# Kernel tuning notes

Measured on AMD Instinct MI355X. Metric: run time of the kernel, lower is better.

## Reference

```python
import jax, jax.numpy as jnp
import numpy as np

N, NN, NI, ND, NH = 20000, 32, 128, 128, 8
RADIUS = 1.0
EPS = 1e-5


def _mlp(x, W1, b1, W2, b2):
    return jax.nn.elu(x @ W1 + b1) @ W2 + b2


def setup_inputs() -> dict:
    key = jax.random.key(0)
    ks = jax.random.split(key, 32)
    s = 0.05
    inp = {
        "features": jax.random.normal(ks[0], (N, NI), jnp.float32),
        "x": jax.random.normal(ks[1], (N, 3), jnp.float32),
        "nuv": jax.random.normal(ks[2], (N, 3, 3), jnp.float32),
        "topk": jax.random.randint(ks[3], (N, NN), 0, N, jnp.int64),
        # query_f: Ni -> Nd -> Nh*Nd
        "qW1": jax.random.normal(ks[4], (NI, ND), jnp.float32) * s,
        "qb1": jnp.zeros((ND,), jnp.float32),
        "qW2": jax.random.normal(ks[5], (ND, NH * ND), jnp.float32) * s,
        "qb2": jnp.zeros((NH * ND,), jnp.float32),
        # geo_encoder: 12 -> Nd -> Nd
        "gW1": jax.random.normal(ks[6], (12, ND), jnp.float32) * s,
        "gb1": jnp.zeros((ND,), jnp.float32),
        "gW2": jax.random.normal(ks[7], (ND, ND), jnp.float32) * s,
        "gb2": jnp.zeros((ND,), jnp.float32),
        # key_f / value_f: Nd -> Nd -> Nd
        "kW1": jax.random.normal(ks[8], (ND, ND), jnp.float32) * s,
        "kb1": jnp.zeros((ND,), jnp.float32),
        "kW2": jax.random.normal(ks[9], (ND, ND), jnp.float32) * s,
        "kb2": jnp.zeros((ND,), jnp.float32),
        "vW1": jax.random.normal(ks[10], (ND, ND), jnp.float32) * s,
        "vb1": jnp.zeros((ND,), jnp.float32),
        "vW2": jax.random.normal(ks[11], (ND, ND), jnp.float32) * s,
        "vb2": jnp.zeros((ND,), jnp.float32),
        # decode_f: Nh*Nd -> Nd -> Nd
        "dW1": jax.random.normal(ks[12], (NH * ND, ND), jnp.float32) * s,
        "db1": jnp.zeros((ND,), jnp.float32),
        "dW2": jax.random.normal(ks[13], (ND, ND), jnp.float32) * s,
        "db2": jnp.zeros((ND,), jnp.float32),
        # LayerNorm
        "ln_g": jnp.ones((ND,), jnp.float32),
        "ln_b": jnp.zeros((ND,), jnp.float32),
    }
    return inp


def reference(features, x, nuv, topk, qW1, qb1, qW2, qb2, gW1, gb1, gW2, gb2,
              kW1, kb1, kW2, kb2, vW1, vb1, vW2, vb2, dW1, db1, dW2, db2,
              ln_g, ln_b):
    n, nn = topk.shape
    sdk = jnp.sqrt(jnp.float32(ND))

    Q = _mlp(features, qW1, qb1, qW2, qb2).reshape(n, NH, ND)  # (N,Nh,Nd)

    features_nn = features[topk]              # (N,nn,Nd)
    x_nn = x[topk]                            # (N,nn,3)
    orient_x = x_nn - x[:, None, :]           # (N,nn,3)
    nuv_nn = nuv[topk].reshape(n, nn * 3, 3)  # (N,nn*3,3)

    dis2 = jnp.sum(orient_x * orient_x, axis=2, keepdims=True)
    dis = jnp.exp(-dis2 / (2.0 * RADIUS * RADIUS))  # (N,nn,1)

    # rotate neighbor offsets / frames into local frame: nuv @ v^T, then transpose
    RL_x = jnp.einsum('nij,nkj->nki', nuv, orient_x)            # (N,nn,3)
    RL_nuv = jnp.einsum('nij,nkj->nki', nuv, nuv_nn)            # (N,nn*3,3)
    RL_nuv = RL_nuv.reshape(n, nn, 9)
    RL = jnp.concatenate([RL_x, RL_nuv], axis=-1)               # (N,nn,12)

    geo_fea = _mlp(RL, gW1, gb1, gW2, gb2)
    geo_fea = dis * geo_fea * features_nn                       # (N,nn,Nd)

    K = _mlp(geo_fea, kW1, kb1, kW2, kb2)                       # (N,nn,Nd)
    V = _mlp(geo_fea, vW1, vb1, vW2, vb2)                       # (N,nn,Nd)

    Mq = jnp.einsum('nhd,nkd->nhk', Q, K)                       # (N,Nh,nn)
    mask = (topk == 0)[:, None, :]                              # (N,1,nn)
    Mq = jnp.where(mask, -jnp.inf, Mq)
    Mq = jax.nn.softmax(Mq / sdk, axis=2)

    out = jnp.einsum('nhk,nkd->nhd', Mq, V).reshape(n, NH * ND)
    out = _mlp(out, dW1, db1, dW2, db2) + features

    mu = jnp.mean(out, axis=-1, keepdims=True)
    var = jnp.var(out, axis=-1, keepdims=True)
    return (out - mu) / jnp.sqrt(var + EPS) * ln_g + ln_b
```

## Files before the change

kernel.cpp:

```cpp
#include <hip/hip_runtime.h>
#include <math.h>
#include <stdint.h>

#define ND 128
#define NNB 32
#define NH 8

typedef __attribute__((ext_vector_type(8))) short bf16x8;
typedef __attribute__((ext_vector_type(4))) float f32x4;
typedef __attribute__((ext_vector_type(8))) unsigned short u16x8;
typedef __attribute__((ext_vector_type(2))) unsigned int u32x2;
typedef unsigned short u16;
typedef unsigned int u32;
typedef unsigned long long u64;

#define OFF_QW1T 0ULL
#define OFF_QW2T 32768ULL
#define OFF_GW1T 294912ULL
#define OFF_GW2T 303104ULL
#define OFF_KW1T 335872ULL
#define OFF_KW2T 368640ULL
#define OFF_VW1T 401408ULL
#define OFF_VW2T 434176ULL
#define OFF_DW1T 466944ULL
#define OFF_DW2T 729088ULL
#define OFF_Q    761856ULL
#define OFF_ATT  (OFF_Q + 20096ULL * 2048ULL)

#define SBAR() asm volatile("s_waitcnt lgkmcnt(0)\n\ts_barrier" ::: "memory")

__device__ __forceinline__ u16 rneb(float f){
    u32 u = __builtin_bit_cast(u32, f);
    u32 r = u + 0x7fffu + ((u >> 16) & 1u);
    return (u16)(r >> 16);
}
__device__ __forceinline__ float elu_f(float v){ return v > 0.f ? v : (__expf(v) - 1.f); }

__device__ __forceinline__ u32 cvtpk(float a, float b){
    u32 r;
    asm("v_cvt_pk_bf16_f32 %0, %1, %2" : "=v"(r) : "v"(a), "v"(b));
    return r;
}
__device__ __forceinline__ u32x2 cvt4(float a, float b, float c, float d){
    u32x2 r; r.x = cvtpk(a, b); r.y = cvtpk(c, d); return r;
}

#define GLDS16(g, l) __builtin_amdgcn_global_load_lds( \
    (const __attribute__((address_space(1))) u32*)(g), \
    (__attribute__((address_space(3))) u32*)(u32)(u64)(l), 16, 0, 0)

__device__ __forceinline__ bf16x8 ldfrag(const u16* base, int row, int kb, int l){
    int r = row + (l & 15);
    int byte = (r << 8) + (((kb << 1) + ((l >> 4) << 4)) ^ ((r & 7) << 4));
    return *(const bf16x8*)((const char*)base + byte);
}
__device__ __forceinline__ bf16x8 ldfragRL(const u16* base, int row, int l){
    int r = row + (l & 15);
    int byte = (r << 6) + ((((l >> 4) << 4)) ^ ((r & 3) << 4));
    return *(const bf16x8*)((const char*)base + byte);
}
__device__ __forceinline__ bf16x8 ldfragG(const char* __restrict__ Wt, int n, int kstride, int kb, int l){
    return *(const bf16x8*)(Wt + (size_t)(n + (l & 15)) * (size_t)kstride
                               + (size_t)((kb << 1) + ((l >> 4) << 4)));
}

__device__ __forceinline__ void gemm2x4(const char* __restrict__ Wt, int kstride, int kbase,
                                        const u16* B, f32x4 acc[2][4], int m0, int n0, int l){
    bf16x8 aw[4][2];
    #pragma unroll
    for (int kk = 0; kk < 4; kk++)
        #pragma unroll
        for (int i = 0; i < 2; i++)
            aw[kk][i] = ldfragG(Wt, m0 + i * 16, kstride, kbase + kk * 32, l);
    __builtin_amdgcn_s_setprio(1);
    #pragma unroll
    for (int kk = 0; kk < 4; kk++){
        #pragma unroll
        for (int nt = 0; nt < 4; nt++){
            bf16x8 b = ldfrag(B, n0 + nt * 16, kk * 32, l);
            #pragma unroll
            for (int mt = 0; mt < 2; mt++)
                acc[mt][nt] = __builtin_amdgcn_mfma_f32_16x16x32_bf16(aw[kk][mt], b, acc[mt][nt], 0, 0, 0);
        }
    }
    __builtin_amdgcn_s_setprio(0);
}

__device__ __forceinline__ void bias_init2(f32x4 acc[2][4], const float* __restrict__ bias,
                                           int m0, int hi){
    #pragma unroll
    for (int mt = 0; mt < 2; mt++){
        float4 bq = *(const float4*)&bias[m0 + mt * 16 + (hi << 2)];
        #pragma unroll
        for (int nt = 0; nt < 4; nt++)
            acc[mt][nt] = (f32x4){bq.x, bq.y, bq.z, bq.w};
    }
}

struct PrepDesc {
    const float* src[10];
    u64 dstoff[10];
    int N[10], Ksrc[10], Kdst[10];
};

__global__ __launch_bounds__(256) void prep_weights(PrepDesc d, char* ws){
    int tid = blockIdx.x * 256 + threadIdx.x;
    #pragma unroll 1
    for (int m = 0; m < 10; m++){
        int cnt = (d.Kdst[m] * d.N[m]) >> 3;
        if (tid < cnt){
            int N = d.N[m];
            int nn = tid % N, k8 = tid / N;
            const float* s = d.src[m];
            u16x8 pk;
            #pragma unroll
            for (int i = 0; i < 8; i++){
                int k = k8 * 8 + i;
                pk[i] = (k < d.Ksrc[m]) ? rneb(s[(size_t)k * N + nn]) : (u16)0;
            }
            *(u16x8*)(ws + d.dstoff[m] + (u64)nn * (u64)(d.Kdst[m] * 2) + (u64)(k8 * 16)) = pk;
            return;
        }
        tid -= cnt;
    }
}

__global__ __launch_bounds__(512, 2) void qmlp_kernel(
    const float* __restrict__ F, const float* __restrict__ qb1, const float* __restrict__ qb2,
    const char* __restrict__ ws, u16* __restrict__ Qg, int n)
{
    __shared__ __align__(16) u16 sIn[16384];
    __shared__ __align__(16) u16 sH[16384];
    const int t = threadIdx.x;
    const int row0 = blockIdx.x * 128;
    const int l = t & 63, w = t >> 6;
    const int m0 = (w & 3) * 32, n0 = (w >> 2) * 64;
    const int hi = l >> 4;

    for (int i = t; i < 4096; i += 512){
        int r = i >> 5, c = (i & 31) * 4;
        int gr = row0 + r;
        float4 v = make_float4(0.f, 0.f, 0.f, 0.f);
        if (gr < n) v = *(const float4*)&F[(size_t)gr * ND + c];
        *(u32x2*)((char*)sIn + (r << 8) + (((c << 1)) ^ ((r & 7) << 4))) = cvt4(v.x, v.y, v.z, v.w);
    }
    SBAR();

    {
        f32x4 acc[2][4];
        bias_init2(acc, qb1, m0, hi);
        gemm2x4(ws + OFF_QW1T, 256, 0, sIn, acc, m0, n0, l);
        #pragma unroll
        for (int mt = 0; mt < 2; mt++){
            int ch0 = m0 + mt * 16 + (hi << 2);
            #pragma unroll
            for (int nt = 0; nt < 4; nt++){
                int row = n0 + nt * 16 + (l & 15);
                *(u32x2*)((char*)sH + (row << 8) + (((ch0 << 1)) ^ ((row & 7) << 4))) =
                    cvt4(elu_f(acc[mt][nt][0]), elu_f(acc[mt][nt][1]),
                         elu_f(acc[mt][nt][2]), elu_f(acc[mt][nt][3]));
            }
        }
    }
    SBAR();

    for (int ct = 0; ct < 8; ct++){
        f32x4 a2[2][4];
        bias_init2(a2, qb2 + ct * 128, m0, hi);
        gemm2x4(ws + OFF_QW2T + (u64)ct * 32768ULL, 256, 0, sH, a2, m0, n0, l);
        #pragma unroll
        for (int mt = 0; mt < 2; mt++){
            int ch0 = m0 + mt * 16 + (hi << 2);
            #pragma unroll
            for (int nt = 0; nt < 4; nt++){
                int row = n0 + nt * 16 + (l & 15);
                int gr = row0 + row;
                if (gr < n)
                    *(u64*)((char*)Qg + (size_t)gr * 2048 + (size_t)((ct * 128 + ch0) * 2)) =
                        __builtin_bit_cast(u64, cvt4(a2[mt][nt][0], a2[mt][nt][1],
                                                     a2[mt][nt][2], a2[mt][nt][3]));
            }
        }
    }
}

template<int ACT, bool INPLACE>
__device__ __forceinline__ void layer2(
    const u16* inB, u16* outB, const char* __restrict__ Wt,
    const float* __restrict__ bias, const float* __restrict__ F,
    const int* sidx, const float* sdis)
{
    const int t = threadIdx.x, l = t & 63, w = t >> 6;
    const int m0 = (w & 3) * 32, n0 = (w >> 2) * 64;
    const int hi = l >> 4;
    f32x4 acc[2][4];
    bias_init2(acc, bias, m0, hi);
    float4 fv[2][4]; float dsc[4];
    if (ACT == 2){
        #pragma unroll
        for (int nt = 0; nt < 4; nt++){
            int row = n0 + nt * 16 + (l & 15);
            int ix = sidx[row];
            dsc[nt] = sdis[row];
            #pragma unroll
            for (int mt = 0; mt < 2; mt++)
                fv[mt][nt] = *(const float4*)&F[(size_t)ix * ND + m0 + mt * 16 + (hi << 2)];
        }
    }
    gemm2x4(Wt, 256, 0, inB, acc, m0, n0, l);
    if (INPLACE) SBAR();
    #pragma unroll
    for (int mt = 0; mt < 2; mt++){
        int ch0 = m0 + mt * 16 + (hi << 2);
        #pragma unroll
        for (int nt = 0; nt < 4; nt++){
            int row = n0 + nt * 16 + (l & 15);
            float v0 = acc[mt][nt][0], v1 = acc[mt][nt][1];
            float v2 = acc[mt][nt][2], v3 = acc[mt][nt][3];
            if (ACT == 1){ v0 = elu_f(v0); v1 = elu_f(v1); v2 = elu_f(v2); v3 = elu_f(v3); }
            if (ACT == 2){
                float s = dsc[nt];
                v0 *= s * fv[mt][nt].x; v1 *= s * fv[mt][nt].y;
                v2 *= s * fv[mt][nt].z; v3 *= s * fv[mt][nt].w;
            }
            *(u32x2*)((char*)outB + (row << 8) + (((ch0 << 1)) ^ ((row & 7) << 4))) =
                cvt4(v0, v1, v2, v3);
        }
    }
    SBAR();
}

__global__ __launch_bounds__(512, 2) void attn_kernel(
    const float* __restrict__ F, const float* __restrict__ X,
    const float* __restrict__ NUV, const int* __restrict__ TOPK,
    const float* __restrict__ gb1, const float* __restrict__ gb2,
    const float* __restrict__ kb1, const float* __restrict__ kb2,
    const float* __restrict__ vb1, const float* __restrict__ vb2,
    const char* __restrict__ ws, const u16* __restrict__ Qg, u16* __restrict__ ATT)
{
    __shared__ __align__(16) u16 bufA[16384];
    __shared__ __align__(16) u16 bufB[16384];
    __shared__ __align__(16) u16 sP16[4096];
    __shared__ float sdis[128];
    __shared__ int   sidx[128];

    const int t = threadIdx.x;
    const int pid0 = blockIdx.x * 4;
    const int l = t & 63, w = t >> 6;
    const int m0 = (w & 3) * 32, n0 = (w >> 2) * 64;
    const int hi = l >> 4;

    if (t < 128){
        int p = t >> 5, k = t & 31;
        int pid = pid0 + p;
        int idx = TOPK[(size_t)pid * NNB + k];
        sidx[t] = idx;
        float x0 = X[(size_t)pid * 3 + 0], x1 = X[(size_t)pid * 3 + 1], x2 = X[(size_t)pid * 3 + 2];
        float ox = X[(size_t)idx * 3 + 0] - x0;
        float oy = X[(size_t)idx * 3 + 1] - x1;
        float oz = X[(size_t)idx * 3 + 2] - x2;
        sdis[t] = __expf(-0.5f * (ox * ox + oy * oy + oz * oz));
        float nv[9];
        #pragma unroll
        for (int i = 0; i < 9; i++) nv[i] = NUV[(size_t)pid * 9 + i];
        float f[12];
        #pragma unroll
        for (int i = 0; i < 3; i++)
            f[i] = nv[i * 3 + 0] * ox + nv[i * 3 + 1] * oy + nv[i * 3 + 2] * oz;
        #pragma unroll
        for (int r = 0; r < 3; r++){
            float a0 = NUV[(size_t)idx * 9 + r * 3 + 0];
            float a1 = NUV[(size_t)idx * 9 + r * 3 + 1];
            float a2 = NUV[(size_t)idx * 9 + r * 3 + 2];
            #pragma unroll
            for (int i = 0; i < 3; i++)
                f[3 + r * 3 + i] = nv[i * 3 + 0] * a0 + nv[i * 3 + 1] * a1 + nv[i * 3 + 2] * a2;
        }
        char* rb = (char*)bufB + (t << 6);
        u32 key = (u32)(t & 3) << 4;
        *(u32x2*)(rb + (0u ^ key))  = cvt4(f[0], f[1], f[2], f[3]);
        *(u32x2*)(rb + (8u ^ key))  = cvt4(f[4], f[5], f[6], f[7]);
        *(u32x2*)(rb + (16u ^ key)) = cvt4(f[8], f[9], f[10], f[11]);
        *(u32x2*)(rb + (24u ^ key)) = (u32x2){0u, 0u};
        *(u32x2*)(rb + (32u ^ key)) = (u32x2){0u, 0u};
        *(u32x2*)(rb + (40u ^ key)) = (u32x2){0u, 0u};
        *(u32x2*)(rb + (48u ^ key)) = (u32x2){0u, 0u};
        *(u32x2*)(rb + (56u ^ key)) = (u32x2){0u, 0u};
    }
    SBAR();

    {
        bf16x8 ag[2];
        #pragma unroll
        for (int i = 0; i < 2; i++) ag[i] = ldfragG(ws + OFF_GW1T, m0 + i * 16, 64, 0, l);
        f32x4 acc[2][4];
        bias_init2(acc, gb1, m0, hi);
        __builtin_amdgcn_s_setprio(1);
        #pragma unroll
        for (int nt = 0; nt < 4; nt++){
            bf16x8 bg = ldfragRL(bufB, n0 + nt * 16, l);
            #pragma unroll
            for (int mt = 0; mt < 2; mt++)
                acc[mt][nt] = __builtin_amdgcn_mfma_f32_16x16x32_bf16(ag[mt], bg, acc[mt][nt], 0, 0, 0);
        }
        __builtin_amdgcn_s_setprio(0);
        #pragma unroll
        for (int mt = 0; mt < 2; mt++){
            int ch0 = m0 + mt * 16 + (hi << 2);
            #pragma unroll
            for (int nt = 0; nt < 4; nt++){
                int row = n0 + nt * 16 + (l & 15);
                *(u32x2*)((char*)bufA + (row << 8) + (((ch0 << 1)) ^ ((row & 7) << 4))) =
                    cvt4(elu_f(acc[mt][nt][0]), elu_f(acc[mt][nt][1]),
                         elu_f(acc[mt][nt][2]), elu_f(acc[mt][nt][3]));
            }
        }
    }
    SBAR();

    layer2<2, false>(bufA, bufB, ws + OFF_GW2T, gb2, F, sidx, sdis);
    layer2<1, false>(bufB, bufA, ws + OFF_KW1T, kb1, F, sidx, sdis);
    layer2<0, true >(bufA, bufA, ws + OFF_KW2T, kb2, F, sidx, sdis);

    if (w < 4){
        f32x4 s0, s1;
        s0 = 0.f; s1 = 0.f;
        const char* qb = (const char*)Qg + (size_t)(pid0 + w) * 2048
                       + (size_t)(l & 7) * 256 + (size_t)(hi << 4);
        #pragma unroll
        for (int kk = 0; kk < 4; kk++){
            bf16x8 bq = *(const bf16x8*)(qb + kk * 64);
            bf16x8 a0 = ldfrag(bufA, w * 32,      kk * 32, l);
            bf16x8 a1 = ldfrag(bufA, w * 32 + 16, kk * 32, l);
            s0 = __builtin_amdgcn_mfma_f32_16x16x32_bf16(a0, bq, s0, 0, 0, 0);
            s1 = __builtin_amdgcn_mfma_f32_16x16x32_bf16(a1, bq, s1, 0, 0, 0);
        }
        const float RS = 0.08838834764831845f;
        float sv[8];
        #pragma unroll
        for (int mt = 0; mt < 2; mt++)
            #pragma unroll
            for (int j = 0; j < 4; j++){
                int kidx = mt * 16 + (hi << 2) + j;
                float x = (mt ? s1[j] : s0[j]) * RS;
                if (sidx[w * 32 + kidx] == 0) x = -INFINITY;
                sv[mt * 4 + j] = x;
            }
        float mx = sv[0];
        #pragma unroll
        for (int i = 1; i < 8; i++) mx = fmaxf(mx, sv[i]);
        mx = fmaxf(mx, __shfl_xor(mx, 16));
        mx = fmaxf(mx, __shfl_xor(mx, 32));
        float e[8], sum = 0.f;
        #pragma unroll
        for (int i = 0; i < 8; i++){ e[i] = __expf(sv[i] - mx); sum += e[i]; }
        sum += __shfl_xor(sum, 16);
        sum += __shfl_xor(sum, 32);
        float inv = 1.f / sum;
        int h = l & 15;
        u32 key = (u32)(h & 3) << 4;
        char* pb = (char*)sP16 + w * 1024 + h * 64;
        *(u32x2*)(pb + (((u32)(hi * 8)) ^ key)) =
            cvt4(e[0] * inv, e[1] * inv, e[2] * inv, e[3] * inv);
        *(u32x2*)(pb + (((u32)(32 + hi * 8)) ^ key)) =
            cvt4(e[4] * inv, e[5] * inv, e[6] * inv, e[7] * inv);
    }
    SBAR();

    layer2<1, false>(bufB, bufA, ws + OFF_VW1T, vb1, F, sidx, sdis);

    {
        const int n0v = (w & 3) * 32, mb = (w >> 2) * 64;
        f32x4 a2[4][2];
        #pragma unroll
        for (int ntb = 0; ntb < 2; ntb++){
            float bv = vb2[n0v + ntb * 16 + (l & 15)];
            #pragma unroll
            for (int mt = 0; mt < 4; mt++)
                a2[mt][ntb] = (f32x4){bv, bv, bv, bv};
        }
        bf16x8 bw[4][2];
        #pragma unroll
        for (int kk = 0; kk < 4; kk++)
            #pragma unroll
            for (int i = 0; i < 2; i++)
                bw[kk][i] = ldfragG(ws + OFF_VW2T, n0v + i * 16, 256, kk * 32, l);
        __builtin_amdgcn_s_setprio(1);
        #pragma unroll
        for (int kk = 0; kk < 4; kk++){
            #pragma unroll
            for (int mt = 0; mt < 4; mt++){
                bf16x8 a = ldfrag(bufA, mb + mt * 16, kk * 32, l);
                #pragma unroll
                for (int ntb = 0; ntb < 2; ntb++)
                    a2[mt][ntb] = __builtin_amdgcn_mfma_f32_16x16x32_bf16(a, bw[kk][ntb], a2[mt][ntb], 0, 0, 0);
            }
        }
        __builtin_amdgcn_s_setprio(0);
        #pragma unroll
        for (int mt = 0; mt < 4; mt++){
            int kv0 = mb + mt * 16 + (hi << 2);
            #pragma unroll
            for (int ntb = 0; ntb < 2; ntb++){
                int ch = n0v + ntb * 16 + (l & 15);
                *(u32x2*)((char*)bufB + (ch << 8) + (((kv0 << 1)) ^ ((ch & 7) << 4))) =
                    cvt4(a2[mt][ntb][0], a2[mt][ntb][1], a2[mt][ntb][2], a2[mt][ntb][3]);
            }
        }
    }
    SBAR();

    {
        const int p = w & 3, dh = (w >> 2) * 64;
        int pid = pid0 + p;
        int h = l & 15;
        bf16x8 pb = *(const bf16x8*)((const char*)sP16 + p * 1024 + h * 64
                                     + (((u32)(hi * 16)) ^ ((u32)(h & 3) << 4)));
        u32 key = ((u32)pid & 7) << 4;
        char* dst = (char*)ATT + (size_t)pid * 2048;
        #pragma unroll
        for (int nt = 0; nt < 4; nt++){
            f32x4 o;
            o = 0.f;
            bf16x8 av = ldfrag(bufB, dh + nt * 16, p * 32, l);
            o = __builtin_amdgcn_mfma_f32_16x16x32_bf16(av, pb, o, 0, 0, 0);
            if (h < 8){
                u32 dbyte = (u32)(dh * 2 + nt * 32 + hi * 8);
                *(u32x2*)(dst + h * 256 + (dbyte ^ key)) = cvt4(o[0], o[1], o[2], o[3]);
            }
        }
    }
}

__global__ __launch_bounds__(512, 2) void decode_kernel(
    const u16* __restrict__ ATT,
    const float* __restrict__ db1, const float* __restrict__ db2,
    const float* __restrict__ F,
    const float* __restrict__ lng, const float* __restrict__ lnb,
    const char* __restrict__ ws, float* __restrict__ OUT, int n)
{
    __shared__ __align__(16) char SM[67584];
    u16* sA = (u16*)SM;
    u16* sH = (u16*)(SM + 32768);
    float* sO = (float*)SM;

    const int t = threadIdx.x;
    const int row0 = blockIdx.x * 128;
    const int l = t & 63, w = t >> 6;
    const int m0 = (w & 3) * 32, n0 = (w >> 2) * 64;
    const int hi = l >> 4;

    f32x4 acc[2][4];
    bias_init2(acc, db1, m0, hi);
    for (int kc = 0; kc < 8; kc++){
        {
            const int seg = (t & 15) * 16, rr = t >> 4;
            const char* g = (const char*)ATT + (size_t)row0 * 2048 + kc * 256;
            #pragma unroll
            for (int i = 0; i < 4; i++){
                int row = i * 32 + rr;
                GLDS16(g + (size_t)row * 2048 + seg, (char*)sA + row * 256 + seg);
            }
        }
        __syncthreads();
        gemm2x4(ws + OFF_DW1T, 2048, kc * 128, sA, acc, m0, n0, l);
        SBAR();
    }
    #pragma unroll
    for (int mt = 0; mt < 2; mt++){
        int ch0 = m0 + mt * 16 + (hi << 2);
        #pragma unroll
        for (int nt = 0; nt < 4; nt++){
            int row = n0 + nt * 16 + (l & 15);
            *(u32x2*)((char*)sH + (row << 8) + (((ch0 << 1)) ^ ((row & 7) << 4))) =
                cvt4(elu_f(acc[mt][nt][0]), elu_f(acc[mt][nt][1]),
                     elu_f(acc[mt][nt][2]), elu_f(acc[mt][nt][3]));
        }
    }
    SBAR();

    f32x4 a2[2][4];
    bias_init2(a2, db2, m0, hi);
    gemm2x4(ws + OFF_DW2T, 256, 0, sH, a2, m0, n0, l);
    SBAR();

    #pragma unroll
    for (int mt = 0; mt < 2; mt++){
        int ch0 = m0 + mt * 16 + (hi << 2);
        #pragma unroll
        for (int nt = 0; nt < 4; nt++){
            int row = n0 + nt * 16 + (l & 15);
            int gr = row0 + row;
            float4 fres = make_float4(0.f, 0.f, 0.f, 0.f);
            if (gr < n) fres = *(const float4*)&F[(size_t)gr * ND + ch0];
            float4 ov = make_float4(a2[mt][nt][0] + fres.x, a2[mt][nt][1] + fres.y,
                                    a2[mt][nt][2] + fres.z, a2[mt][nt][3] + fres.w);
            *(float4*)&sO[row * 132 + ch0] = ov;
        }
    }
    SBAR();

    {
        int r = t >> 2, q = t & 3;
        const float* rowp = sO + r * 132 + q * 32;
        float s = 0.f;
        #pragma unroll
        for (int i = 0; i < 8; i++){
            float4 v = ((const float4*)rowp)[i];
            s += v.x + v.y + v.z + v.w;
        }
        s += __shfl_xor(s, 1);
        s += __shfl_xor(s, 2);
        float mu = s * (1.0f / 128.0f);
        float q2 = 0.f;
        #pragma unroll
        for (int i = 0; i < 8; i++){
            float4 v = ((const float4*)rowp)[i];
            q2 += (v.x - mu) * (v.x - mu) + (v.y - mu) * (v.y - mu)
                + (v.z - mu) * (v.z - mu) + (v.w - mu) * (v.w - mu);
        }
        q2 += __shfl_xor(q2, 1);
        q2 += __shfl_xor(q2, 2);
        float rstd = rsqrtf(q2 * (1.0f / 128.0f) + 1e-5f);
        int gr = row0 + r;
        if (gr < n){
            #pragma unroll
            for (int i = 0; i < 8; i++){
                float4 v = ((const float4*)rowp)[i];
                int c = q * 32 + i * 4;
                float4 g4 = *(const float4*)&lng[c];
                float4 b4 = *(const float4*)&lnb[c];
                float4 ov = make_float4((v.x - mu) * rstd * g4.x + b4.x,
                                        (v.y - mu) * rstd * g4.y + b4.y,
                                        (v.z - mu) * rstd * g4.z + b4.z,
                                        (v.w - mu) * rstd * g4.w + b4.w);
                *(float4*)&OUT[(size_t)gr * ND + c] = ov;
            }
        }
    }
}

extern "C" void kernel_launch(void* const* d_in, const int* in_sizes, int n_in,
                              void* d_out, int out_size, void* d_ws, size_t ws_size,
                              hipStream_t stream)
{
    const float* F    = (const float*)d_in[0];
    const float* X    = (const float*)d_in[1];
    const float* NUV  = (const float*)d_in[2];
    const int*   TOPK = (const int*)d_in[3];
    const float* qW1  = (const float*)d_in[4];
    const float* qb1  = (const float*)d_in[5];
    const float* qW2  = (const float*)d_in[6];
    const float* qb2  = (const float*)d_in[7];
    const float* gW1  = (const float*)d_in[8];
    const float* gb1  = (const float*)d_in[9];
    const float* gW2  = (const float*)d_in[10];
    const float* gb2  = (const float*)d_in[11];
    const float* kW1  = (const float*)d_in[12];
    const float* kb1  = (const float*)d_in[13];
    const float* kW2  = (const float*)d_in[14];
    const float* kb2  = (const float*)d_in[15];
    const float* vW1  = (const float*)d_in[16];
    const float* vb1  = (const float*)d_in[17];
    const float* vW2  = (const float*)d_in[18];
    const float* vb2  = (const float*)d_in[19];
    const float* dW1  = (const float*)d_in[20];
    const float* db1  = (const float*)d_in[21];
    const float* dW2  = (const float*)d_in[22];
    const float* db2  = (const float*)d_in[23];
    const float* lng  = (const float*)d_in[24];
    const float* lnb  = (const float*)d_in[25];

    const int n = in_sizes[0] / ND;
    char* wsb = (char*)d_ws;

    PrepDesc pd;
    const float* srcs[10] = {qW1, qW2, gW1, gW2, kW1, kW2, vW1, vW2, dW1, dW2};
    u64 offs[10] = {OFF_QW1T, OFF_QW2T, OFF_GW1T, OFF_GW2T, OFF_KW1T,
                    OFF_KW2T, OFF_VW1T, OFF_VW2T, OFF_DW1T, OFF_DW2T};
    int Ns[10]   = {128, 1024, 128, 128, 128, 128, 128, 128, 128, 128};
    int Ksrc[10] = {128, 128, 12, 128, 128, 128, 128, 128, 1024, 128};
    int Kdst[10] = {128, 128, 32, 128, 128, 128, 128, 128, 1024, 128};
    for (int i = 0; i < 10; i++){
        pd.src[i] = srcs[i]; pd.dstoff[i] = offs[i];
        pd.N[i] = Ns[i]; pd.Ksrc[i] = Ksrc[i]; pd.Kdst[i] = Kdst[i];
    }
    prep_weights<<<186, 256, 0, stream>>>(pd, wsb);

    u16* Qg  = (u16*)(wsb + OFF_Q);
    u16* ATT = (u16*)(wsb + OFF_ATT);
    const int nb = (n + 127) / 128;

    qmlp_kernel<<<nb, 512, 0, stream>>>(F, qb1, qb2, wsb, Qg, n);
    attn_kernel<<<n / 4, 512, 0, stream>>>(F, X, NUV, TOPK, gb1, gb2,
                                           kb1, kb2, vb1, vb2, wsb, Qg, ATT);
    decode_kernel<<<nb, 512, 0, stream>>>(ATT, db1, db2, F, lng, lnb, wsb, (float*)d_out, n);
}
```

Measured before the change: 451.3 us.

## Make attention kernel persistent with register-resident weights and 4-wave blocks

```diff
diff --git a/kernel.cpp b/kernel.cpp
--- a/kernel.cpp
+++ b/kernel.cpp
@@ -64,23 +64,16 @@
                                + (size_t)((kb << 1) + ((l >> 4) << 4)));
 }
 
-__device__ __forceinline__ void gemm2x4(const char* __restrict__ Wt, int kstride, int kbase,
-                                        const u16* B, f32x4 acc[2][4], int m0, int n0, int l){
-    bf16x8 aw[4][2];
-    #pragma unroll
-    for (int kk = 0; kk < 4; kk++)
-        #pragma unroll
-        for (int i = 0; i < 2; i++)
-            aw[kk][i] = ldfragG(Wt, m0 + i * 16, kstride, kbase + kk * 32, l);
+__device__ __forceinline__ void gemm_half(const bf16x8 aw[4][2], const u16* B,
+                                          int nbase, f32x4 acc[2][4], int l){
     __builtin_amdgcn_s_setprio(1);
     #pragma unroll
     for (int kk = 0; kk < 4; kk++){
         #pragma unroll
         for (int nt = 0; nt < 4; nt++){
-            bf16x8 b = ldfrag(B, n0 + nt * 16, kk * 32, l);
-            #pragma unroll
-            for (int mt = 0; mt < 2; mt++)
-                acc[mt][nt] = __builtin_amdgcn_mfma_f32_16x16x32_bf16(aw[kk][mt], b, acc[mt][nt], 0, 0, 0);
+            bf16x8 b = ldfrag(B, nbase + nt * 16, kk * 32, l);
+            acc[0][nt] = __builtin_amdgcn_mfma_f32_16x16x32_bf16(aw[kk][0], b, acc[0][nt], 0, 0, 0);
+            acc[1][nt] = __builtin_amdgcn_mfma_f32_16x16x32_bf16(aw[kk][1], b, acc[1][nt], 0, 0, 0);
         }
     }
     __builtin_amdgcn_s_setprio(0);
@@ -95,6 +88,52 @@
         for (int nt = 0; nt < 4; nt++)
             acc[mt][nt] = (f32x4){bq.x, bq.y, bq.z, bq.w};
     }
+}
+
+template<int ACT, bool INPLACE>
+__device__ __forceinline__ void layerP(
+    const u16* inB, u16* outB, const bf16x8 aw[4][2],
+    const float* __restrict__ bias, const float* __restrict__ F,
+    const int* sidx, const float* sdis, int m0, int l, int hi)
+{
+    #pragma unroll
+    for (int half = 0; half < 2; half++){
+        const int nbase = half * 64;
+        float4 fv[2][4]; float ds[4];
+        if (ACT == 2){
+            #pragma unroll
+            for (int nt = 0; nt < 4; nt++){
+                int row = nbase + nt * 16 + (l & 15);
+                int ix = sidx[row];
+                ds[nt] = sdis[row];
+                fv[0][nt] = *(const float4*)&F[(size_t)ix * ND + m0 + (hi << 2)];
+                fv[1][nt] = *(const float4*)&F[(size_t)ix * ND + m0 + 16 + (hi << 2)];
+            }
+        }
+        f32x4 acc[2][4];
+        bias_init2(acc, bias, m0, hi);
+        gemm_half(aw, inB, nbase, acc, l);
+        if (INPLACE) SBAR();
+        #pragma unroll
+        for (int mt = 0; mt < 2; mt++){
+            int ch0 = m0 + mt * 16 + (hi << 2);
+            #pragma unroll
+            for (int nt = 0; nt < 4; nt++){
+                int row = nbase + nt * 16 + (l & 15);
+                float v0 = acc[mt][nt][0], v1 = acc[mt][nt][1];
+                float v2 = acc[mt][nt][2], v3 = acc[mt][nt][3];
+                if (ACT == 1){ v0 = elu_f(v0); v1 = elu_f(v1); v2 = elu_f(v2); v3 = elu_f(v3); }
+                if (ACT == 2){
+                    float s = ds[nt];
+                    v0 *= s * fv[mt][nt].x; v1 *= s * fv[mt][nt].y;
+                    v2 *= s * fv[mt][nt].z; v3 *= s * fv[mt][nt].w;
+                }
+                *(u32x2*)((char*)outB + (row << 8) + (((ch0 << 1)) ^ ((row & 7) << 4))) =
+                    cvt4(v0, v1, v2, v3);
+            }
+        }
+    }
+    SBAR();
 }
 
 struct PrepDesc {
@@ -123,6 +162,28 @@
         }
         tid -= cnt;
     }
+}
+
+__device__ __forceinline__ void gemm2x4G(const char* __restrict__ Wt, int kstride, int kbase,
+                                         const u16* B, f32x4 acc[2][4], int m0, int n0, int l){
+    bf16x8 aw[4][2];
+    #pragma unroll
+    for (int kk = 0; kk < 4; kk++)
+        #pragma unroll
+        for (int i = 0; i < 2; i++)
+            aw[kk][i] = ldfragG(Wt, m0 + i * 16, kstride, kbase + kk * 32, l);
+    __builtin_amdgcn_s_setprio(1);
+    #pragma unroll
+    for (int kk = 0; kk < 4; kk++){
+        #pragma unroll
+        for (int nt = 0; nt < 4; nt++){
+            bf16x8 b = ldfrag(B, n0 + nt * 16, kk * 32, l);
+            #pragma unroll
+            for (int mt = 0; mt < 2; mt++)
+                acc[mt][nt] = __builtin_amdgcn_mfma_f32_16x16x32_bf16(aw[kk][mt], b, acc[mt][nt], 0, 0, 0);
+        }
+    }
+    __builtin_amdgcn_s_setprio(0);
 }
 
 __global__ __launch_bounds__(512, 2) void qmlp_kernel(
@@ -149,7 +210,7 @@
     {
         f32x4 acc[2][4];
         bias_init2(acc, qb1, m0, hi);
-        gemm2x4(ws + OFF_QW1T, 256, 0, sIn, acc, m0, n0, l);
+        gemm2x4G(ws + OFF_QW1T, 256, 0, sIn, acc, m0, n0, l);
         #pragma unroll
         for (int mt = 0; mt < 2; mt++){
             int ch0 = m0 + mt * 16 + (hi << 2);
@@ -167,7 +228,7 @@
     for (int ct = 0; ct < 8; ct++){
         f32x4 a2[2][4];
         bias_init2(a2, qb2 + ct * 128, m0, hi);
-        gemm2x4(ws + OFF_QW2T + (u64)ct * 32768ULL, 256, 0, sH, a2, m0, n0, l);
+        gemm2x4G(ws + OFF_QW2T + (u64)ct * 32768ULL, 256, 0, sH, a2, m0, n0, l);
         #pragma unroll
         for (int mt = 0; mt < 2; mt++){
             int ch0 = m0 + mt * 16 + (hi << 2);
@@ -184,249 +245,216 @@
     }
 }
 
-template<int ACT, bool INPLACE>
-__device__ __forceinline__ void layer2(
-    const u16* inB, u16* outB, const char* __restrict__ Wt,
-    const float* __restrict__ bias, const float* __restrict__ F,
-    const int* sidx, const float* sdis)
-{
-    const int t = threadIdx.x, l = t & 63, w = t >> 6;
-    const int m0 = (w & 3) * 32, n0 = (w >> 2) * 64;
-    const int hi = l >> 4;
-    f32x4 acc[2][4];
-    bias_init2(acc, bias, m0, hi);
-    float4 fv[2][4]; float dsc[4];
-    if (ACT == 2){
-        #pragma unroll
-        for (int nt = 0; nt < 4; nt++){
-            int row = n0 + nt * 16 + (l & 15);
-            int ix = sidx[row];
-            dsc[nt] = sdis[row];
-            #pragma unroll
-            for (int mt = 0; mt < 2; mt++)
-                fv[mt][nt] = *(const float4*)&F[(size_t)ix * ND + m0 + mt * 16 + (hi << 2)];
-        }
-    }
-    gemm2x4(Wt, 256, 0, inB, acc, m0, n0, l);
-    if (INPLACE) SBAR();
-    #pragma unroll
-    for (int mt = 0; mt < 2; mt++){
-        int ch0 = m0 + mt * 16 + (hi << 2);
-        #pragma unroll
-        for (int nt = 0; nt < 4; nt++){
-            int row = n0 + nt * 16 + (l & 15);
-            float v0 = acc[mt][nt][0], v1 = acc[mt][nt][1];
-            float v2 = acc[mt][nt][2], v3 = acc[mt][nt][3];
-            if (ACT == 1){ v0 = elu_f(v0); v1 = elu_f(v1); v2 = elu_f(v2); v3 = elu_f(v3); }
-            if (ACT == 2){
-                float s = dsc[nt];
-                v0 *= s * fv[mt][nt].x; v1 *= s * fv[mt][nt].y;
-                v2 *= s * fv[mt][nt].z; v3 *= s * fv[mt][nt].w;
-            }
-            *(u32x2*)((char*)outB + (row << 8) + (((ch0 << 1)) ^ ((row & 7) << 4))) =
-                cvt4(v0, v1, v2, v3);
-        }
-    }
-    SBAR();
-}
-
-__global__ __launch_bounds__(512, 2) void attn_kernel(
+__global__ __launch_bounds__(256, 2) void attn_kernel(
     const float* __restrict__ F, const float* __restrict__ X,
     const float* __restrict__ NUV, const int* __restrict__ TOPK,
     const float* __restrict__ gb1, const float* __restrict__ gb2,
     const float* __restrict__ kb1, const float* __restrict__ kb2,
     const float* __restrict__ vb1, const float* __restrict__ vb2,
-    const char* __restrict__ ws, const u16* __restrict__ Qg, u16* __restrict__ ATT)
+    const char* __restrict__ ws, const u16* __restrict__ Qg, u16* __restrict__ ATT,
+    int ngroups)
 {
     __shared__ __align__(16) u16 bufA[16384];
     __shared__ __align__(16) u16 bufB[16384];
-    __shared__ __align__(16) u16 sP16[4096];
+    __shared__ __align__(16) u16 sP16[2048];
     __shared__ float sdis[128];
     __shared__ int   sidx[128];
 
     const int t = threadIdx.x;
-    const int pid0 = blockIdx.x * 4;
     const int l = t & 63, w = t >> 6;
-    const int m0 = (w & 3) * 32, n0 = (w >> 2) * 64;
+    const int m0 = w * 32;
     const int hi = l >> 4;
 
-    if (t < 128){
-        int p = t >> 5, k = t & 31;
-        int pid = pid0 + p;
-        int idx = TOPK[(size_t)pid * NNB + k];
-        sidx[t] = idx;
-        float x0 = X[(size_t)pid * 3 + 0], x1 = X[(size_t)pid * 3 + 1], x2 = X[(size_t)pid * 3 + 2];
-        float ox = X[(size_t)idx * 3 + 0] - x0;
-        float oy = X[(size_t)idx * 3 + 1] - x1;
-        float oz = X[(size_t)idx * 3 + 2] - x2;
-        sdis[t] = __expf(-0.5f * (ox * ox + oy * oy + oz * oz));
-        float nv[9];
-        #pragma unroll
-        for (int i = 0; i < 9; i++) nv[i] = NUV[(size_t)pid * 9 + i];
-        float f[12];
-        #pragma unroll
-        for (int i = 0; i < 3; i++)
-            f[i] = nv[i * 3 + 0] * ox + nv[i * 3 + 1] * oy + nv[i * 3 + 2] * oz;
-        #pragma unroll
-        for (int r = 0; r < 3; r++){
-            float a0 = NUV[(size_t)idx * 9 + r * 3 + 0];
-            float a1 = NUV[(size_t)idx * 9 + r * 3 + 1];
-            float a2 = NUV[(size_t)idx * 9 + r * 3 + 2];
+    bf16x8 ag[2];
+    #pragma unroll
+    for (int i = 0; i < 2; i++)
+        ag[i] = *(const bf16x8*)(ws + OFF_GW1T
+                 + (u64)((m0 + i * 16 + (l & 15)) * 64 + (hi << 4)));
+    bf16x8 wg2[4][2], wk1[4][2], wk2[4][2], wv1[4][2], wv2[4][2];
+    #pragma unroll
+    for (int kk = 0; kk < 4; kk++)
+        #pragma unroll
+        for (int i = 0; i < 2; i++){
+            u64 fo = (u64)((m0 + i * 16 + (l & 15)) * 256 + kk * 64 + (hi << 4));
+            wg2[kk][i] = *(const bf16x8*)(ws + OFF_GW2T + fo);
+            wk1[kk][i] = *(const bf16x8*)(ws + OFF_KW1T + fo);
+            wk2[kk][i] = *(const bf16x8*)(ws + OFF_KW2T + fo);
+            wv1[kk][i] = *(const bf16x8*)(ws + OFF_VW1T + fo);
+            wv2[kk][i] = *(const bf16x8*)(ws + OFF_VW2T + fo);
+        }
+
+    for (int g = blockIdx.x; g < ngroups; g += gridDim.x){
+        const int pid0 = g * 4;
+        SBAR();
+
+        if (t < 128){
+            int p = t >> 5, k = t & 31;
+            int pid = pid0 + p;
+            int idx = TOPK[(size_t)pid * NNB + k];
+            sidx[t] = idx;
+            float x0 = X[(size_t)pid * 3 + 0], x1 = X[(size_t)pid * 3 + 1], x2 = X[(size_t)pid * 3 + 2];
+            float ox = X[(size_t)idx * 3 + 0] - x0;
+            float oy = X[(size_t)idx * 3 + 1] - x1;
+            float oz = X[(size_t)idx * 3 + 2] - x2;
+            sdis[t] = __expf(-0.5f * (ox * ox + oy * oy + oz * oz));
+            float nv[9];
+            #pragma unroll
+            for (int i = 0; i < 9; i++) nv[i] = NUV[(size_t)pid * 9 + i];
+            float f[12];
             #pragma unroll
             for (int i = 0; i < 3; i++)
-                f[3 + r * 3 + i] = nv[i * 3 + 0] * a0 + nv[i * 3 + 1] * a1 + nv[i * 3 + 2] * a2;
-        }
-        char* rb = (char*)bufB + (t << 6);
-        u32 key = (u32)(t & 3) << 4;
-        *(u32x2*)(rb + (0u ^ key))  = cvt4(f[0], f[1], f[2], f[3]);
-        *(u32x2*)(rb + (8u ^ key))  = cvt4(f[4], f[5], f[6], f[7]);
-        *(u32x2*)(rb + (16u ^ key)) = cvt4(f[8], f[9], f[10], f[11]);
-        *(u32x2*)(rb + (24u ^ key)) = (u32x2){0u, 0u};
-        *(u32x2*)(rb + (32u ^ key)) = (u32x2){0u, 0u};
-        *(u32x2*)(rb + (40u ^ key)) = (u32x2){0u, 0u};
-        *(u32x2*)(rb + (48u ^ key)) = (u32x2){0u, 0u};
-        *(u32x2*)(rb + (56u ^ key)) = (u32x2){0u, 0u};
-    }
-    SBAR();
-
-    {
-        bf16x8 ag[2];
-        #pragma unroll
-        for (int i = 0; i < 2; i++) ag[i] = ldfragG(ws + OFF_GW1T, m0 + i * 16, 64, 0, l);
-        f32x4 acc[2][4];
-        bias_init2(acc, gb1, m0, hi);
-        __builtin_amdgcn_s_setprio(1);
-        #pragma unroll
-        for (int nt = 0; nt < 4; nt++){
-            bf16x8 bg = ldfragRL(bufB, n0 + nt * 16, l);
+                f[i] = nv[i * 3 + 0] * ox + nv[i * 3 + 1] * oy + nv[i * 3 + 2] * oz;
+            #pragma unroll
+            for (int r = 0; r < 3; r++){
+                float a0 = NUV[(size_t)idx * 9 + r * 3 + 0];
+                float a1 = NUV[(size_t)idx * 9 + r * 3 + 1];
+                float a2 = NUV[(size_t)idx * 9 + r * 3 + 2];
+                #pragma unroll
+                for (int i = 0; i < 3; i++)
+                    f[3 + r * 3 + i] = nv[i * 3 + 0] * a0 + nv[i * 3 + 1] * a1 + nv[i * 3 + 2] * a2;
+            }
+            char* rb = (char*)bufB + (t << 6);
+            u32 key = (u32)(t & 3) << 4;
+            *(u32x2*)(rb + (0u ^ key))  = cvt4(f[0], f[1], f[2], f[3]);
+            *(u32x2*)(rb + (8u ^ key))  = cvt4(f[4], f[5], f[6], f[7]);
+            *(u32x2*)(rb + (16u ^ key)) = cvt4(f[8], f[9], f[10], f[11]);
+            *(u32x2*)(rb + (24u ^ key)) = (u32x2){0u, 0u};
+            *(u32x2*)(rb + (32u ^ key)) = (u32x2){0u, 0u};
+            *(u32x2*)(rb + (40u ^ key)) = (u32x2){0u, 0u};
+            *(u32x2*)(rb + (48u ^ key)) = (u32x2){0u, 0u};
+            *(u32x2*)(rb + (56u ^ key)) = (u32x2){0u, 0u};
+        }
+        SBAR();
+
+        #pragma unroll
+        for (int half = 0; half < 2; half++){
+            f32x4 acc[2][4];
+            bias_init2(acc, gb1, m0, hi);
+            __builtin_amdgcn_s_setprio(1);
+            #pragma unroll
+            for (int nt = 0; nt < 4; nt++){
+                bf16x8 bg = ldfragRL(bufB, half * 64 + nt * 16, l);
+                acc[0][nt] = __builtin_amdgcn_mfma_f32_16x16x32_bf16(ag[0], bg, acc[0][nt], 0, 0, 0);
+                acc[1][nt] = __builtin_amdgcn_mfma_f32_16x16x32_bf16(ag[1], bg, acc[1][nt], 0, 0, 0);
+            }
+            __builtin_amdgcn_s_setprio(0);
+            #pragma unroll
+            for (int mt = 0; mt < 2; mt++){
+                int ch0 = m0 + mt * 16 + (hi << 2);
+                #pragma unroll
+                for (int nt = 0; nt < 4; nt++){
+                    int row = half * 64 + nt * 16 + (l & 15);
+                    *(u32x2*)((char*)bufA + (row << 8) + (((ch0 << 1)) ^ ((row & 7) << 4))) =
+                        cvt4(elu_f(acc[mt][nt][0]), elu_f(acc[mt][nt][1]),
+                             elu_f(acc[mt][nt][2]), elu_f(acc[mt][nt][3]));
+                }
+            }
+        }
+        SBAR();
+
+        layerP<2, false>(bufA, bufB, wg2, gb2, F, sidx, sdis, m0, l, hi);
+        layerP<1, false>(bufB, bufA, wk1, kb1, F, sidx, sdis, m0, l, hi);
+        layerP<0, true >(bufA, bufA, wk2, kb2, F, sidx, sdis, m0, l, hi);
+
+        {
+            f32x4 s0, s1;
+            s0 = 0.f; s1 = 0.f;
+            const char* qb = (const char*)Qg + (size_t)(pid0 + w) * 2048
+                           + (size_t)(l & 7) * 256 + (size_t)(hi << 4);
+            #pragma unroll
+            for (int kk = 0; kk < 4; kk++){
+                bf16x8 bq = *(const bf16x8*)(qb + kk * 64);
+                bf16x8 a0 = ldfrag(bufA, w * 32,      kk * 32, l);
+                bf16x8 a1 = ldfrag(bufA, w * 32 + 16, kk * 32, l);
+                s0 = __builtin_amdgcn_mfma_f32_16x16x32_bf16(a0, bq, s0, 0, 0, 0);
+                s1 = __builtin_amdgcn_mfma_f32_16x16x32_bf16(a1, bq, s1, 0, 0, 0);
+            }
+            const float RS = 0.08838834764831845f;
+            float sv[8];
             #pragma unroll
             for (int mt = 0; mt < 2; mt++)
-                acc[mt][nt] = __builtin_amdgcn_mfma_f32_16x16x32_bf16(ag[mt], bg, acc[mt][nt], 0, 0, 0);
-        }
-        __builtin_amdgcn_s_setprio(0);
-        #pragma unroll
-        for (int mt = 0; mt < 2; mt++){
-            int ch0 = m0 + mt * 16 + (hi << 2);
-            #pragma unroll
-            for (int nt = 0; nt < 4; nt++){
-                int row = n0 + nt * 16 + (l & 15);
-                *(u32x2*)((char*)bufA + (row << 8) + (((ch0 << 1)) ^ ((row & 7) << 4))) =
-                    cvt4(elu_f(acc[mt][nt][0]), elu_f(acc[mt][nt][1]),
-                         elu_f(acc[mt][nt][2]), elu_f(acc[mt][nt][3]));
-            }
-        }
-    }
-    SBAR();
-
-    layer2<2, false>(bufA, bufB, ws + OFF_GW2T, gb2, F, sidx, sdis);
-    layer2<1, false>(bufB, bufA, ws + OFF_KW1T, kb1, F, sidx, sdis);
-    layer2<0, true >(bufA, bufA, ws + OFF_KW2T, kb2, F, sidx, sdis);
-
-    if (w < 4){
-        f32x4 s0, s1;
-        s0 = 0.f; s1 = 0.f;
-        const char* qb = (const char*)Qg + (size_t)(pid0 + w) * 2048
-                       + (size_t)(l & 7) * 256 + (size_t)(hi << 4);
-        #pragma unroll
-        for (int kk = 0; kk < 4; kk++){
-            bf16x8 bq = *(const bf16x8*)(qb + kk * 64);
-            bf16x8 a0 = ldfrag(bufA, w * 32,      kk * 32, l);
-            bf16x8 a1 = ldfrag(bufA, w * 32 + 16, kk * 32, l);
-            s0 = __builtin_amdgcn_mfma_f32_16x16x32_bf16(a0, bq, s0, 0, 0, 0);
-            s1 = __builtin_amdgcn_mfma_f32_16x16x32_bf16(a1, bq, s1, 0, 0, 0);
-        }
-        const float RS = 0.08838834764831845f;
-        float sv[8];
-        #pragma unroll
-        for (int mt = 0; mt < 2; mt++)
-            #pragma unroll
-            for (int j = 0; j < 4; j++){
-                int kidx = mt * 16 + (hi << 2) + j;
-                float x = (mt ? s1[j] : s0[j]) * RS;
-                if (sidx[w * 32 + kidx] == 0) x = -INFINITY;
-                sv[mt * 4 + j] = x;
-            }
-        float mx = sv[0];
-        #pragma unroll
-        for (int i = 1; i < 8; i++) mx = fmaxf(mx, sv[i]);
-        mx = fmaxf(mx, __shfl_xor(mx, 16));
-        mx = fmaxf(mx, __shfl_xor(mx, 32));
-        float e[8], sum = 0.f;
-        #pragma unroll
-        for (int i = 0; i < 8; i++){ e[i] = __expf(sv[i] - mx); sum += e[i]; }
-        sum += __shfl_xor(sum, 16);
-        sum += __shfl_xor(sum, 32);
-        float inv = 1.f / sum;
-        int h = l & 15;
-        u32 key = (u32)(h & 3) << 4;
-        char* pb = (char*)sP16 + w * 1024 + h * 64;
-        *(u32x2*)(pb + (((u32)(hi * 8)) ^ key)) =
-            cvt4(e[0] * inv, e[1] * inv, e[2] * inv, e[3] * inv);
-        *(u32x2*)(pb + (((u32)(32 + hi * 8)) ^ key)) =
-            cvt4(e[4] * inv, e[5] * inv, e[6] * inv, e[7] * inv);
-    }
-    SBAR();
-
-    layer2<1, false>(bufB, bufA, ws + OFF_VW1T, vb1, F, sidx, sdis);
-
-    {
-        const int n0v = (w & 3) * 32, mb = (w >> 2) * 64;
-        f32x4 a2[4][2];
-        #pragma unroll
-        for (int ntb = 0; ntb < 2; ntb++){
-            float bv = vb2[n0v + ntb * 16 + (l & 15)];
-            #pragma unroll
-            for (int mt = 0; mt < 4; mt++)
-                a2[mt][ntb] = (f32x4){bv, bv, bv, bv};
-        }
-        bf16x8 bw[4][2];
-        #pragma unroll
-        for (int kk = 0; kk < 4; kk++)
-            #pragma unroll
-            for (int i = 0; i < 2; i++)
-                bw[kk][i] = ldfragG(ws + OFF_VW2T, n0v + i * 16, 256, kk * 32, l);
-        __builtin_amdgcn_s_setprio(1);
-        #pragma unroll
-        for (int kk = 0; kk < 4; kk++){
-            #pragma unroll
-            for (int mt = 0; mt < 4; mt++){
-                bf16x8 a = ldfrag(bufA, mb + mt * 16, kk * 32, l);
                 #pragma unroll
-                for (int ntb = 0; ntb < 2; ntb++)
-                    a2[mt][ntb] = __builtin_amdgcn_mfma_f32_16x16x32_bf16(a, bw[kk][ntb], a2[mt][ntb], 0, 0, 0);
-            }
-        }
-        __builtin_amdgcn_s_setprio(0);
-        #pragma unroll
-        for (int mt = 0; mt < 4; mt++){
-            int kv0 = mb + mt * 16 + (hi << 2);
-            #pragma unroll
-            for (int ntb = 0; ntb < 2; ntb++){
-                int ch = n0v + ntb * 16 + (l & 15);
-                *(u32x2*)((char*)bufB + (ch << 8) + (((kv0 << 1)) ^ ((ch & 7) << 4))) =
-                    cvt4(a2[mt][ntb][0], a2[mt][ntb][1], a2[mt][ntb][2], a2[mt][ntb][3]);
-            }
-        }
-    }
-    SBAR();
-
-    {
-        const int p = w & 3, dh = (w >> 2) * 64;
-        int pid = pid0 + p;
-        int h = l & 15;
-        bf16x8 pb = *(const bf16x8*)((const char*)sP16 + p * 1024 + h * 64
-                                     + (((u32)(hi * 16)) ^ ((u32)(h & 3) << 4)));
-        u32 key = ((u32)pid & 7) << 4;
-        char* dst = (char*)ATT + (size_t)pid * 2048;
-        #pragma unroll
-        for (int nt = 0; nt < 4; nt++){
-            f32x4 o;
-            o = 0.f;
-            bf16x8 av = ldfrag(bufB, dh + nt * 16, p * 32, l);
-            o = __builtin_amdgcn_mfma_f32_16x16x32_bf16(av, pb, o, 0, 0, 0);
-            if (h < 8){
-                u32 dbyte = (u32)(dh * 2 + nt * 32 + hi * 8);
-                *(u32x2*)(dst + h * 256 + (dbyte ^ key)) = cvt4(o[0], o[1], o[2], o[3]);
+                for (int j = 0; j < 4; j++){
+                    int kidx = mt * 16 + (hi << 2) + j;
+                    float x = (mt ? s1[j] : s0[j]) * RS;
+                    if (sidx[w * 32 + kidx] == 0) x = -INFINITY;
+                    sv[mt * 4 + j] = x;
+                }
+            float mx = sv[0];
+            #pragma unroll
+            for (int i = 1; i < 8; i++) mx = fmaxf(mx, sv[i]);
+            mx = fmaxf(mx, __shfl_xor(mx, 16));
+            mx = fmaxf(mx, __shfl_xor(mx, 32));
+            float e[8], sum = 0.f;
+            #pragma unroll
+            for (int i = 0; i < 8; i++){ e[i] = __expf(sv[i] - mx); sum += e[i]; }
+            sum += __shfl_xor(sum, 16);
+            sum += __shfl_xor(sum, 32);
+            float inv = 1.f / sum;
+            int h = l & 15;
+            u32 key = (u32)(h & 3) << 4;
+            char* pb = (char*)sP16 + w * 1024 + h * 64;
+            *(u32x2*)(pb + (((u32)(hi * 8)) ^ key)) =
+                cvt4(e[0] * inv, e[1] * inv, e[2] * inv, e[3] * inv);
+            *(u32x2*)(pb + (((u32)(32 + hi * 8)) ^ key)) =
+                cvt4(e[4] * inv, e[5] * inv, e[6] * inv, e[7] * inv);
+        }
+        SBAR();
+
+        layerP<1, false>(bufB, bufA, wv1, vb1, F, sidx, sdis, m0, l, hi);
+
+        #pragma unroll
+        for (int half = 0; half < 2; half++){
+            f32x4 a2[4][2];
+            #pragma unroll
+            for (int ntc = 0; ntc < 2; ntc++){
+                float bv = vb2[m0 + ntc * 16 + (l & 15)];
+                #pragma unroll
+                for (int mtr = 0; mtr < 4; mtr++)
+                    a2[mtr][ntc] = (f32x4){bv, bv, bv, bv};
+            }
+            __builtin_amdgcn_s_setprio(1);
+            #pragma unroll
+            for (int kk = 0; kk < 4; kk++){
+                #pragma unroll
+                for (int mtr = 0; mtr < 4; mtr++){
+                    bf16x8 a = ldfrag(bufA, half * 64 + mtr * 16, kk * 32, l);
+                    #pragma unroll
+                    for (int ntc = 0; ntc < 2; ntc++)
+                        a2[mtr][ntc] = __builtin_amdgcn_mfma_f32_16x16x32_bf16(a, wv2[kk][ntc], a2[mtr][ntc], 0, 0, 0);
+                }
+            }
+            __builtin_amdgcn_s_setprio(0);
+            #pragma unroll
+            for (int mtr = 0; mtr < 4; mtr++){
+                int kv0 = half * 64 + mtr * 16 + (hi << 2);
+                #pragma unroll
+                for (int ntc = 0; ntc < 2; ntc++){
+                    int ch = m0 + ntc * 16 + (l & 15);
+                    *(u32x2*)((char*)bufB + (ch << 8) + (((kv0 << 1)) ^ ((ch & 7) << 4))) =
+                        cvt4(a2[mtr][ntc][0], a2[mtr][ntc][1], a2[mtr][ntc][2], a2[mtr][ntc][3]);
+                }
+            }
+        }
+        SBAR();
+
+        {
+            int pid = pid0 + w;
+            int h = l & 15;
+            bf16x8 pb = *(const bf16x8*)((const char*)sP16 + w * 1024 + h * 64
+                                         + (((u32)(hi * 16)) ^ ((u32)(h & 3) << 4)));
+            u32 key = ((u32)pid & 7) << 4;
+            char* dst = (char*)ATT + (size_t)pid * 2048;
+            #pragma unroll
+            for (int nt = 0; nt < 8; nt++){
+                f32x4 o;
+                o = 0.f;
+                bf16x8 av = ldfrag(bufB, nt * 16, w * 32, l);
+                o = __builtin_amdgcn_mfma_f32_16x16x32_bf16(av, pb, o, 0, 0, 0);
+                if (h < 8){
+                    u32 dbyte = (u32)(nt * 32 + hi * 8);
+                    *(u32x2*)(dst + h * 256 + (dbyte ^ key)) = cvt4(o[0], o[1], o[2], o[3]);
+                }
             }
         }
     }
@@ -463,7 +491,7 @@
             }
         }
         __syncthreads();
-        gemm2x4(ws + OFF_DW1T, 2048, kc * 128, sA, acc, m0, n0, l);
+        gemm2x4G(ws + OFF_DW1T, 2048, kc * 128, sA, acc, m0, n0, l);
         SBAR();
     }
     #pragma unroll
@@ -481,7 +509,7 @@
 
     f32x4 a2[2][4];
     bias_init2(a2, db2, m0, hi);
-    gemm2x4(ws + OFF_DW2T, 256, 0, sH, a2, m0, n0, l);
+    gemm2x4G(ws + OFF_DW2T, 256, 0, sH, a2, m0, n0, l);
     SBAR();
 
     #pragma unroll
@@ -590,9 +618,10 @@
     u16* Qg  = (u16*)(wsb + OFF_Q);
     u16* ATT = (u16*)(wsb + OFF_ATT);
     const int nb = (n + 127) / 128;
+    const int ngroups = n / 4;
 
     qmlp_kernel<<<nb, 512, 0, stream>>>(F, qb1, qb2, wsb, Qg, n);
-    attn_kernel<<<n / 4, 512, 0, stream>>>(F, X, NUV, TOPK, gb1, gb2,
-                                           kb1, kb2, vb1, vb2, wsb, Qg, ATT);
+    attn_kernel<<<512, 256, 0, stream>>>(F, X, NUV, TOPK, gb1, gb2,
+                                         kb1, kb2, vb1, vb2, wsb, Qg, ATT, ngroups);
     decode_kernel<<<nb, 512, 0, stream>>>(ATT, db1, db2, F, lng, lnb, wsb, (float*)d_out, n);
 }
```

After: 393.3 us, median of 2. -12.8%, faster.
